# Kernel optimization log

Hardware: AMD Instinct MI355X
Metric: run time of the kernel (lower is better)

## Reference

```python
import jax, jax.numpy as jnp
import numpy as np

B, C, H, W = 4, 384, 128, 128
HEADS = 8
EPS = 1e-12  # torch F.normalize default eps


def setup_inputs() -> dict:
    key = jax.random.key(0)
    k1, k2, k3, k4 = jax.random.split(key, 4)
    in1 = jax.random.normal(k1, (B, C, H, W), dtype=jnp.float32)
    in2 = jax.random.normal(k2, (B, C, H, W), dtype=jnp.float32)
    temperature = jnp.ones((HEADS, 1, 1), dtype=jnp.float32)
    proj_w = jax.random.normal(k3, (C, C), dtype=jnp.float32) * (1.0 / np.sqrt(C))
    proj_b = jax.random.normal(k4, (C,), dtype=jnp.float32) * 0.01
    return {"in1": in1, "in2": in2, "temperature": temperature,
            "proj_w": proj_w, "proj_b": proj_b}


def _l2norm_last(x):
    # torch F.normalize(dim=-1): x / max(||x||_2, eps)
    n = jnp.sqrt(jnp.sum(x * x, axis=-1, keepdims=True))
    return x / jnp.maximum(n, EPS)


def reference(in1, in2, temperature, proj_w, proj_b):
    b, c, h, w = in1.shape
    hd = c // HEADS  # per-head channels
    # b (head c) h w -> b head c (h w)
    q = in1.reshape(b, HEADS, hd, h * w)
    k = in2.reshape(b, HEADS, hd, h * w)
    q = _l2norm_last(q)
    k = _l2norm_last(k)
    # channel attention: [b, head, hd, hd]
    attn = jnp.einsum('bhcn,bhdn->bhcd', q, k) * temperature[None]
    attn = jax.nn.softmax(attn, axis=-1)
    out = jnp.einsum('bhcd,bhdn->bhcn', attn, k)  # [b, head, hd, HW]
    out = out.reshape(b, c, h, w)
    # 1x1 conv projection
    out = jnp.einsum('oc,bchw->bohw', proj_w, out) + proj_b[None, :, None, None]
    return out
```

## Files before the change

### kernel.cpp

```cpp
#include <hip/hip_runtime.h>
#include <hip/hip_bf16.h>

#define NB 4
#define CC 384
#define HEADS 8
#define HD 48
#define NN 16384
#define NROWS (NB*CC)

typedef __attribute__((ext_vector_type(8))) short bf16x8;
typedef __attribute__((ext_vector_type(4))) float f32x4;

__device__ __forceinline__ unsigned short f2bf(float f) {
  __hip_bfloat16 h = __float2bfloat16(f);
  return __builtin_bit_cast(unsigned short, h);
}
__device__ __forceinline__ unsigned int packbf(float a, float b) {
  return (unsigned int)f2bf(a) | ((unsigned int)f2bf(b) << 16);
}

__global__ __launch_bounds__(256) void k_gram(
    const float* __restrict__ in1, const float* __restrict__ in2,
    float* __restrict__ partial, float* __restrict__ sumsq_part)
{
  int bh = blockIdx.x;
  int chunk = blockIdx.y;
  int wave = threadIdx.x >> 6, lane = threadIdx.x & 63;
  int b = bh >> 3, h = bh & 7;
  size_t base = ((size_t)(b*CC + h*HD)) * NN;
  int lrow = lane & 15, lk = (lane >> 4) << 3;
  int kstart = chunk*512 + wave*128;
  f32x4 acc[3][3] = {};
  float sq[3] = {0.f,0.f,0.f}, sk[3] = {0.f,0.f,0.f};
  for (int ks = 0; ks < 4; ++ks) {
    int kpos = kstart + ks*32 + lk;
    bf16x8 a[3], bb[3];
    #pragma unroll
    for (int t = 0; t < 3; ++t) {
      int rr = t*16 + lrow;
      const float* pq = in1 + base + (size_t)rr * NN + kpos;
      const float* pk = in2 + base + (size_t)rr * NN + kpos;
      float4 q0 = *(const float4*)pq, q1 = *((const float4*)pq + 1);
      float4 k0 = *(const float4*)pk, k1 = *((const float4*)pk + 1);
      union { bf16x8 v; unsigned short u[8]; } ua, ub;
      ua.u[0]=f2bf(q0.x); ua.u[1]=f2bf(q0.y); ua.u[2]=f2bf(q0.z); ua.u[3]=f2bf(q0.w);
      ua.u[4]=f2bf(q1.x); ua.u[5]=f2bf(q1.y); ua.u[6]=f2bf(q1.z); ua.u[7]=f2bf(q1.w);
      ub.u[0]=f2bf(k0.x); ub.u[1]=f2bf(k0.y); ub.u[2]=f2bf(k0.z); ub.u[3]=f2bf(k0.w);
      ub.u[4]=f2bf(k1.x); ub.u[5]=f2bf(k1.y); ub.u[6]=f2bf(k1.z); ub.u[7]=f2bf(k1.w);
      a[t] = ua.v; bb[t] = ub.v;
      sq[t] += q0.x*q0.x + q0.y*q0.y + q0.z*q0.z + q0.w*q0.w
             + q1.x*q1.x + q1.y*q1.y + q1.z*q1.z + q1.w*q1.w;
      sk[t] += k0.x*k0.x + k0.y*k0.y + k0.z*k0.z + k0.w*k0.w
             + k1.x*k1.x + k1.y*k1.y + k1.z*k1.z + k1.w*k1.w;
    }
    #pragma unroll
    for (int i = 0; i < 3; ++i)
      #pragma unroll
      for (int j = 0; j < 3; ++j)
        acc[i][j] = __builtin_amdgcn_mfma_f32_16x16x32_bf16(a[i], bb[j], acc[i][j], 0, 0, 0);
  }
  __shared__ float red[4][HD][HD+1];
  __shared__ float sqs[4][96];
  #pragma unroll
  for (int t = 0; t < 3; ++t) {
    float s = sq[t]; s += __shfl_xor(s, 16); s += __shfl_xor(s, 32);
    if (lane < 16) sqs[wave][t*16 + lane] = s;
    float s2 = sk[t]; s2 += __shfl_xor(s2, 16); s2 += __shfl_xor(s2, 32);
    if (lane < 16) sqs[wave][48 + t*16 + lane] = s2;
  }
  #pragma unroll
  for (int i = 0; i < 3; ++i)
    #pragma unroll
    for (int j = 0; j < 3; ++j)
      #pragma unroll
      for (int m = 0; m < 4; ++m) {
        int rr = i*16 + (lane>>4)*4 + m;
        int cc2 = j*16 + (lane&15);
        red[wave][rr][cc2] = acc[i][j][m];
      }
  __syncthreads();
  float* pout = partial + ((size_t)bh*32 + chunk) * (HD*HD);
  for (int e = threadIdx.x; e < HD*HD; e += 256) {
    int r = e / HD, c = e % HD;
    pout[e] = red[0][r][c] + red[1][r][c] + red[2][r][c] + red[3][r][c];
  }
  if (threadIdx.x < 96) {
    float* sout = sumsq_part + ((size_t)bh*32 + chunk) * 96;
    sout[threadIdx.x] = sqs[0][threadIdx.x] + sqs[1][threadIdx.x]
                      + sqs[2][threadIdx.x] + sqs[3][threadIdx.x];
  }
}

__global__ __launch_bounds__(256) void k_redsm(
    const float* __restrict__ partial, const float* __restrict__ sumsq_part,
    const float* __restrict__ temp, float* __restrict__ attn_out,
    float* __restrict__ rinv_k_g)
{
  int bh = blockIdx.x; int b = bh >> 3, h = bh & 7;
  __shared__ float attn[HD][HD+1];
  __shared__ float rqs[HD], rks[HD];
  if (threadIdx.x < 96) {
    float s = 0.f;
    #pragma unroll
    for (int c = 0; c < 32; ++c)
      s += sumsq_part[((size_t)bh*32 + c)*96 + threadIdx.x];
    float rinv = 1.f / fmaxf(sqrtf(s), 1e-12f);
    if (threadIdx.x < 48) rqs[threadIdx.x] = rinv;
    else { rks[threadIdx.x-48] = rinv; rinv_k_g[b*CC + h*HD + threadIdx.x-48] = rinv; }
  }
  const float* p = partial + (size_t)bh * 32 * (HD*HD);
  float tscale = temp[h];
  __syncthreads();
  for (int e = threadIdx.x; e < HD*HD; e += 256) {
    float s = 0.f;
    #pragma unroll
    for (int c2 = 0; c2 < 32; ++c2) s += p[c2*(HD*HD) + e];
    attn[e/HD][e%HD] = s * tscale * rqs[e/HD] * rks[e%HD];
  }
  __syncthreads();
  if (threadIdx.x < HD) {
    float* rowp = attn[threadIdx.x];
    float m = rowp[0];
    for (int j = 1; j < HD; ++j) m = fmaxf(m, rowp[j]);
    float sum = 0.f;
    for (int j = 0; j < HD; ++j) { float e = expf(rowp[j]-m); rowp[j] = e; sum += e; }
    float inv = 1.f / sum;
    for (int j = 0; j < HD; ++j) rowp[j] *= inv;
  }
  __syncthreads();
  float* ao = attn_out + (size_t)bh * (HD*HD);
  for (int e = threadIdx.x; e < HD*HD; e += 256)
    ao[e] = attn[e/HD][e%HD];
}

__global__ __launch_bounds__(256) void k_m(
    const float* __restrict__ attn, const float* __restrict__ proj_w,
    const float* __restrict__ rinv_k, unsigned short* __restrict__ Mbf)
{
  int b = blockIdx.x, ot = blockIdx.y;
  int o0 = ot * 16;
  __shared__ float sw[16*CC];
  __shared__ float sa[HEADS*HD*HD];
  const float* ab = attn + (size_t)b * HEADS * HD * HD;
  for (int i = threadIdx.x; i < HEADS*HD*HD; i += 256) sa[i] = ab[i];
  for (int i = threadIdx.x; i < 16*CC; i += 256)
    sw[i] = proj_w[(size_t)(o0 + i/CC)*CC + (i%CC)];
  __syncthreads();
  for (int idx = threadIdx.x; idx < 16*96; idx += 256) {
    int o = idx / 96, c4 = idx % 96;
    int col = c4 * 4;
    int h = col / HD, d = col % HD;
    const float* wp = sw + o*CC + h*HD;
    const float* ap = sa + h*HD*HD + d;
    f32x4 s = {0.f, 0.f, 0.f, 0.f};
    #pragma unroll
    for (int c2 = 0; c2 < HD; ++c2) {
      float w = wp[c2];
      f32x4 av = *(const f32x4*)(ap + c2*HD);
      s += w * av;
    }
    f32x4 rk = *(const f32x4*)(rinv_k + b*CC + col);
    s *= rk;
    ushort4 o4;
    o4.x = f2bf(s[0]); o4.y = f2bf(s[1]); o4.z = f2bf(s[2]); o4.w = f2bf(s[3]);
    *(ushort4*)(Mbf + ((size_t)b*CC + o0 + o)*CC + col) = o4;
  }
}

#define BM 128
#define BN 128
#define BK 64

__global__ __launch_bounds__(256) void k_final(
    const float* __restrict__ in2, const unsigned short* __restrict__ Mbf,
    const float* __restrict__ bias, float* __restrict__ out)
{
  int b = blockIdx.z;
  int bm = blockIdx.y * BM, bn = blockIdx.x * BN;
  int tid = threadIdx.x, lane = tid & 63, wave = tid >> 6;
  int wrow = wave >> 1, wcol = wave & 1;
  __shared__ unsigned short Bt[BN * BK];
  char* btb = (char*)Bt;
  const float* kb = in2 + (size_t)b * CC * NN;
  const unsigned short* Mb = Mbf + (size_t)b * CC * CC;
  f32x4 acc[4][4] = {};
  int lrow = lane & 15, lkg = lane >> 4;
  for (int k0 = 0; k0 < CC; k0 += BK) {
    #pragma unroll
    for (int s = 0; s < 2; ++s) {
      int slot = tid + s*256;
      int cp = slot >> 4;
      int ng = slot & 15;
      int n0 = ng * 8;
      int c = k0 + cp*2;
      const float* p0 = kb + (size_t)c*NN + bn + n0;
      const float* p1 = kb + (size_t)(c+1)*NN + bn + n0;
      float4 a0 = *(const float4*)p0, a1 = *((const float4*)p0 + 1);
      float4 b0 = *(const float4*)p1, b1 = *((const float4*)p1 + 1);
      float lo[8] = {a0.x,a0.y,a0.z,a0.w,a1.x,a1.y,a1.z,a1.w};
      float hi[8] = {b0.x,b0.y,b0.z,b0.w,b1.x,b1.y,b1.z,b1.w};
      #pragma unroll
      for (int i = 0; i < 8; ++i) {
        int n = n0 + i;
        unsigned int val = packbf(lo[i], hi[i]);
        int pc = (cp>>2) ^ (n & 7) ^ ((n >> 3) & 7);
        *(unsigned int*)(btb + n*128 + (pc<<4) + ((cp&3)<<2)) = val;
      }
    }
    __syncthreads();
    #pragma unroll
    for (int kk = 0; kk < BK; kk += 32) {
      bf16x8 af[4], bfr[4];
      #pragma unroll
      for (int t = 0; t < 4; ++t) {
        int o = bm + wrow*64 + t*16 + lrow;
        af[t] = *(const bf16x8*)(Mb + (size_t)o*CC + (k0 + kk + (lkg<<3)));
        int n = wcol*64 + t*16 + lrow;
        int lc = (kk>>3) + lkg;
        int pc = lc ^ (n & 7) ^ ((n >> 3) & 7);
        bfr[t] = *(const bf16x8*)(btb + n*128 + (pc<<4));
      }
      #pragma unroll
      for (int i = 0; i < 4; ++i)
        #pragma unroll
        for (int j = 0; j < 4; ++j)
          acc[i][j] = __builtin_amdgcn_mfma_f32_16x16x32_bf16(af[i], bfr[j], acc[i][j], 0, 0, 0);
    }
    __syncthreads();
  }
  #pragma unroll
  for (int i = 0; i < 4; ++i) {
    int obase = bm + wrow*64 + i*16 + lkg*4;
    #pragma unroll
    for (int j = 0; j < 4; ++j) {
      int n = bn + wcol*64 + j*16 + lrow;
      #pragma unroll
      for (int m = 0; m < 4; ++m) {
        int o = obase + m;
        out[((size_t)b*CC + o)*NN + n] = acc[i][j][m] + bias[o];
      }
    }
  }
}

extern "C" void kernel_launch(void* const* d_in, const int* in_sizes, int n_in,
                              void* d_out, int out_size, void* d_ws, size_t ws_size,
                              hipStream_t stream)
{
  const float* in1    = (const float*)d_in[0];
  const float* in2    = (const float*)d_in[1];
  const float* temp   = (const float*)d_in[2];
  const float* proj_w = (const float*)d_in[3];
  const float* proj_b = (const float*)d_in[4];
  float* out = (float*)d_out;
  char* ws = (char*)d_ws;

  size_t off = 0;
  float* partial    = (float*)(ws + off); off += (size_t)32*32*HD*HD*4;
  float* sumsq_part = (float*)(ws + off); off += (size_t)32*32*96*4;
  float* attn_out   = (float*)(ws + off); off += (size_t)32*HD*HD*4;
  float* rinv_k     = (float*)(ws + off); off += NROWS*4;
  unsigned short* Mbf = (unsigned short*)(ws + off);

  k_gram<<<dim3(32, 32), dim3(256), 0, stream>>>(in1, in2, partial, sumsq_part);
  k_redsm<<<dim3(32), dim3(256), 0, stream>>>(partial, sumsq_part, temp, attn_out, rinv_k);
  k_m<<<dim3(NB, 24), dim3(256), 0, stream>>>(attn_out, proj_w, rinv_k, Mbf);
  k_final<<<dim3(NN/BN, CC/BM, NB), dim3(256), 0, stream>>>(in2, Mbf, proj_b, out);
}
```

Before: 142.8 us.

## Stage gram inputs through LDS with coalesced row loads in bf16

The gram kernel now loads q/k rows with fully coalesced float4 reads (each wave reads contiguous 256-element row segments), converts them to bf16 and stores them in LDS. MFMA fragments are then read from LDS instead of strided per-lane global loads. This replaces the earlier pattern where 16 rows per wave were read with 32-byte pieces per lane. Sum-of-squares is now computed from the bf16-rounded values, which slightly changes the norms. The change also adds two barriers per round and a larger LDS footprint, which may reduce occupancy.

```diff
diff --git a/kernel.cpp b/kernel.cpp
--- a/kernel.cpp
+++ b/kernel.cpp
@@ -18,7 +18,12 @@
 __device__ __forceinline__ unsigned int packbf(float a, float b) {
   return (unsigned int)f2bf(a) | ((unsigned int)f2bf(b) << 16);
 }
-
+__device__ __forceinline__ float bf2f(short s) {
+  unsigned int u = ((unsigned int)(unsigned short)s) << 16;
+  return __builtin_bit_cast(float, u);
+}
+
+#define SROW 264
 __global__ __launch_bounds__(256) void k_gram(
     const float* __restrict__ in1, const float* __restrict__ in2,
     float* __restrict__ partial, float* __restrict__ sumsq_part)
@@ -28,66 +33,83 @@
   int wave = threadIdx.x >> 6, lane = threadIdx.x & 63;
   int b = bh >> 3, h = bh & 7;
   size_t base = ((size_t)(b*CC + h*HD)) * NN;
-  int lrow = lane & 15, lk = (lane >> 4) << 3;
-  int kstart = chunk*512 + wave*128;
+  int lrow = lane & 15, lkg = lane >> 4;
+
+  __shared__ char smem[50688];
+  unsigned short* sq_ = (unsigned short*)smem;
+  unsigned short* sk_ = (unsigned short*)(smem + 25344);
+  float* red = (float*)smem;
+  float* sqs = (float*)(smem + 38400);
+
   f32x4 acc[3][3] = {};
-  float sq[3] = {0.f,0.f,0.f}, sk[3] = {0.f,0.f,0.f};
-  for (int ks = 0; ks < 4; ++ks) {
-    int kpos = kstart + ks*32 + lk;
-    bf16x8 a[3], bb[3];
-    #pragma unroll
-    for (int t = 0; t < 3; ++t) {
-      int rr = t*16 + lrow;
-      const float* pq = in1 + base + (size_t)rr * NN + kpos;
-      const float* pk = in2 + base + (size_t)rr * NN + kpos;
-      float4 q0 = *(const float4*)pq, q1 = *((const float4*)pq + 1);
-      float4 k0 = *(const float4*)pk, k1 = *((const float4*)pk + 1);
-      union { bf16x8 v; unsigned short u[8]; } ua, ub;
-      ua.u[0]=f2bf(q0.x); ua.u[1]=f2bf(q0.y); ua.u[2]=f2bf(q0.z); ua.u[3]=f2bf(q0.w);
-      ua.u[4]=f2bf(q1.x); ua.u[5]=f2bf(q1.y); ua.u[6]=f2bf(q1.z); ua.u[7]=f2bf(q1.w);
-      ub.u[0]=f2bf(k0.x); ub.u[1]=f2bf(k0.y); ub.u[2]=f2bf(k0.z); ub.u[3]=f2bf(k0.w);
-      ub.u[4]=f2bf(k1.x); ub.u[5]=f2bf(k1.y); ub.u[6]=f2bf(k1.z); ub.u[7]=f2bf(k1.w);
-      a[t] = ua.v; bb[t] = ub.v;
-      sq[t] += q0.x*q0.x + q0.y*q0.y + q0.z*q0.z + q0.w*q0.w
-             + q1.x*q1.x + q1.y*q1.y + q1.z*q1.z + q1.w*q1.w;
-      sk[t] += k0.x*k0.x + k0.y*k0.y + k0.z*k0.z + k0.w*k0.w
-             + k1.x*k1.x + k1.y*k1.y + k1.z*k1.z + k1.w*k1.w;
-    }
-    #pragma unroll
-    for (int i = 0; i < 3; ++i)
-      #pragma unroll
-      for (int j = 0; j < 3; ++j)
-        acc[i][j] = __builtin_amdgcn_mfma_f32_16x16x32_bf16(a[i], bb[j], acc[i][j], 0, 0, 0);
-  }
-  __shared__ float red[4][HD][HD+1];
-  __shared__ float sqs[4][96];
+  float ssq[3] = {0.f,0.f,0.f}, ssk[3] = {0.f,0.f,0.f};
+
+  for (int rnd = 0; rnd < 2; ++rnd) {
+    int kbase = chunk*512 + rnd*256;
+    #pragma unroll 8
+    for (int rr = 0; rr < 24; ++rr) {
+      int row = wave*24 + rr;
+      int tr = row < 48 ? row : row - 48;
+      const float* src = (row < 48 ? in1 : in2) + base + (size_t)tr*NN + kbase;
+      float4 v = *(const float4*)(src + lane*4);
+      unsigned short* dstp = (row < 48 ? sq_ : sk_) + tr*SROW + lane*4;
+      *(unsigned int*)(dstp)     = packbf(v.x, v.y);
+      *(unsigned int*)(dstp + 2) = packbf(v.z, v.w);
+    }
+    __syncthreads();
+    #pragma unroll
+    for (int ks = 0; ks < 2; ++ks) {
+      int col = wave*64 + ks*32 + lkg*8;
+      bf16x8 a[3], bb[3];
+      #pragma unroll
+      for (int t = 0; t < 3; ++t) {
+        int rr2 = t*16 + lrow;
+        a[t]  = *(const bf16x8*)(sq_ + rr2*SROW + col);
+        bb[t] = *(const bf16x8*)(sk_ + rr2*SROW + col);
+      }
+      #pragma unroll
+      for (int t = 0; t < 3; ++t)
+        #pragma unroll
+        for (int j = 0; j < 8; ++j) {
+          float fa = bf2f(a[t][j]);  ssq[t] += fa*fa;
+          float fb = bf2f(bb[t][j]); ssk[t] += fb*fb;
+        }
+      #pragma unroll
+      for (int i = 0; i < 3; ++i)
+        #pragma unroll
+        for (int j = 0; j < 3; ++j)
+          acc[i][j] = __builtin_amdgcn_mfma_f32_16x16x32_bf16(a[i], bb[j], acc[i][j], 0, 0, 0);
+    }
+    __syncthreads();
+  }
+
+  #pragma unroll
+  for (int i = 0; i < 3; ++i)
+    #pragma unroll
+    for (int j = 0; j < 3; ++j)
+      #pragma unroll
+      for (int m = 0; m < 4; ++m) {
+        int rr2 = i*16 + (lane>>4)*4 + m;
+        int cc2 = j*16 + (lane&15);
+        red[(size_t)wave*2400 + rr2*50 + cc2] = acc[i][j][m];
+      }
   #pragma unroll
   for (int t = 0; t < 3; ++t) {
-    float s = sq[t]; s += __shfl_xor(s, 16); s += __shfl_xor(s, 32);
-    if (lane < 16) sqs[wave][t*16 + lane] = s;
-    float s2 = sk[t]; s2 += __shfl_xor(s2, 16); s2 += __shfl_xor(s2, 32);
-    if (lane < 16) sqs[wave][48 + t*16 + lane] = s2;
-  }
-  #pragma unroll
-  for (int i = 0; i < 3; ++i)
-    #pragma unroll
-    for (int j = 0; j < 3; ++j)
-      #pragma unroll
-      for (int m = 0; m < 4; ++m) {
-        int rr = i*16 + (lane>>4)*4 + m;
-        int cc2 = j*16 + (lane&15);
-        red[wave][rr][cc2] = acc[i][j][m];
-      }
+    float s = ssq[t]; s += __shfl_xor(s, 16); s += __shfl_xor(s, 32);
+    if (lane < 16) sqs[wave*96 + t*16 + lane] = s;
+    float s2 = ssk[t]; s2 += __shfl_xor(s2, 16); s2 += __shfl_xor(s2, 32);
+    if (lane < 16) sqs[wave*96 + 48 + t*16 + lane] = s2;
+  }
   __syncthreads();
   float* pout = partial + ((size_t)bh*32 + chunk) * (HD*HD);
   for (int e = threadIdx.x; e < HD*HD; e += 256) {
     int r = e / HD, c = e % HD;
-    pout[e] = red[0][r][c] + red[1][r][c] + red[2][r][c] + red[3][r][c];
+    pout[e] = red[r*50+c] + red[2400 + r*50+c] + red[4800 + r*50+c] + red[7200 + r*50+c];
   }
   if (threadIdx.x < 96) {
     float* sout = sumsq_part + ((size_t)bh*32 + chunk) * 96;
-    sout[threadIdx.x] = sqs[0][threadIdx.x] + sqs[1][threadIdx.x]
-                      + sqs[2][threadIdx.x] + sqs[3][threadIdx.x];
+    sout[threadIdx.x] = sqs[threadIdx.x] + sqs[96 + threadIdx.x]
+                      + sqs[192 + threadIdx.x] + sqs[288 + threadIdx.x];
   }
 }
 
```

Result: faster. 130.2 us (-8.8%).
